# Optimization experiments

Measured on AMD Instinct MI355X. Metric: run time of the kernel, lower is better.

Reference implementation:

```python
import jax, jax.numpy as jnp
import numpy as np

B, S, V, H = 1, 2048, 1024, 16
D = V // H  # head_size = 64


def setup_inputs() -> dict:
    key = jax.random.key(0)
    ks = jax.random.split(key, 7)
    s = 1.0 / np.sqrt(V)  # keep logits in a sane range
    return {
        "x": jax.random.normal(ks[0], (B, S, V), jnp.float32),
        "W_qkv": (jax.random.normal(ks[1], (3 * V, V), jnp.float32) * s),
        "W_out": (jax.random.normal(ks[2], (V, V), jnp.float32) * s),
        "W_pos": (jax.random.normal(ks[3], (V, V), jnp.float32) * s),
        "u_vec": (jax.random.normal(ks[4], (1, H, 1, D), jnp.float32) * 0.02),
        "v_vec": (jax.random.normal(ks[5], (1, H, 1, D), jnp.float32) * 0.02),
        "rel_embed": jax.random.normal(ks[6], (S, V), jnp.float32),
    }


def reference(x, W_qkv, W_out, W_pos, u_vec, v_vec, rel_embed):
    b, s, _ = x.shape
    # qkv projection (nn.Linear, no bias): x @ W.T, then split into q,k,v
    qkv = x @ W_qkv.T
    q, k, v = jnp.split(qkv, 3, axis=-1)
    to_heads = lambda t: t.reshape(b, s, H, D).transpose(0, 2, 1, 3)  # [B,H,S,D]
    q, k, v = to_heads(q), to_heads(k), to_heads(v)

    # content term: (q + u) @ k^T  -> [B,H,S,S]
    attn_dots = jnp.einsum('bhid,bhjd->bhij', q + u_vec, k)

    # relative-position term: Linear(rel_embed).T viewed as [H, D, S]
    rel = (rel_embed @ W_pos.T).T.reshape(H, D, s)
    query_posn = jnp.einsum('bhid,hdj->bhij', q + v_vec, rel)  # [B,H,S,S]

    # Transformer-XL style shift-gather: out[i, j] = in[i, (j - i - 1) mod S]
    col_idx = ((-jnp.arange(s))[:, None] + jnp.arange(s)[None, :] - 1) % s
    shifted = jnp.take_along_axis(query_posn, col_idx[None, None, :, :], axis=-1)

    causal_mask = jnp.triu(jnp.ones((s, s), dtype=bool), k=1)  # True above diagonal
    dots = jnp.where(causal_mask, -jnp.inf, attn_dots + shifted) / np.sqrt(D)
    scores = jax.nn.softmax(dots, axis=-1)

    attn = jnp.einsum('bhij,bhjd->bhid', scores, v)
    out = attn.transpose(0, 2, 1, 3).reshape(b, s, V) @ W_out.T
    return out
```

## Files before the change

kernel.cpp:

```cpp
#include <hip/hip_runtime.h>
#include <math.h>

#define S 2048
#define H 16
#define D 64
#define V 1024

typedef float f32x4 __attribute__((ext_vector_type(4)));
typedef __bf16 bf16x8 __attribute__((ext_vector_type(8)));
typedef unsigned short u16;

#define GLOBAL_AS __attribute__((address_space(1)))
#define LDS_AS __attribute__((address_space(3)))

__device__ __forceinline__ u16 f2bf(float x) {
    unsigned u = __float_as_uint(x);
    u = u + 0x7FFFu + ((u >> 16) & 1u);
    return (u16)(u >> 16);
}
__device__ __forceinline__ float bf2f(u16 b) {
    return __uint_as_float(((unsigned)b) << 16);
}

#if __has_builtin(__builtin_amdgcn_global_load_lds)
#define HAS_ASYNC 1
#endif

__device__ __forceinline__ void async_ld16(const u16* g, u16* ldsu, int lane) {
#ifdef HAS_ASYNC
    auto gp = reinterpret_cast<GLOBAL_AS void*>(reinterpret_cast<uintptr_t>(g));
    auto lp = reinterpret_cast<LDS_AS void*>(reinterpret_cast<uintptr_t>(ldsu));
    __builtin_amdgcn_global_load_lds(gp, lp, 16, 0, 0);
#else
    *(uint4*)((char*)ldsu + lane * 16) = *(const uint4*)g;
#endif
}

__global__ __launch_bounds__(256) void prep5(
    const float* __restrict__ a0, u16* __restrict__ b0, int n0,
    const float* __restrict__ a1, u16* __restrict__ b1, int n1,
    const float* __restrict__ a2, u16* __restrict__ b2, int n2,
    const float* __restrict__ a3, u16* __restrict__ b3, int n3,
    const float* __restrict__ a4, u16* __restrict__ b4, int n4)
{
    const int tot = n0 + n1 + n2 + n3 + n4;
    for (int i = blockIdx.x * 256 + threadIdx.x; i < tot; i += gridDim.x * 256) {
        const float* s; u16* d; int j = i;
        if (j < n0) { s = a0; d = b0; }
        else if ((j -= n0) < n1) { s = a1; d = b1; }
        else if ((j -= n1) < n2) { s = a2; d = b2; }
        else if ((j -= n2) < n3) { s = a3; d = b3; }
        else { j -= n3; s = a4; d = b4; }
        float4 f = ((const float4*)s)[j];
        ((ushort4*)d)[j] = make_ushort4(f2bf(f.x), f2bf(f.y), f2bf(f.z), f2bf(f.w));
    }
}

__global__ __launch_bounds__(256) void gemm_proj(
    const u16* __restrict__ x_h, const u16* __restrict__ rel_h,
    const u16* __restrict__ Wq_h, const u16* __restrict__ Wpos_h,
    u16* __restrict__ qk_h, u16* __restrict__ Vt_g, u16* __restrict__ P_h)
{
    __shared__ u16 A_s[128 * 32];
    __shared__ u16 B_s[64 * 32];

    const int bid = blockIdx.x;
    const bool g1 = bid < 768;
    const int m0 = (g1 ? (bid / 48) : ((bid - 768) / 16)) * 128;
    const int n0 = (g1 ? (bid % 48) : ((bid - 768) % 16)) * 64;
    const u16* Ag = g1 ? x_h : rel_h;
    const u16* Bg = g1 ? Wq_h : Wpos_h;

    const int tid = threadIdx.x;
    const int lane = tid & 63;
    const int w = tid >> 6;
    const int wm = (w & 1) * 64, wn = (w >> 1) * 32;
    const int fr = lane & 15;
    const int fq = lane >> 4;
    const int lr = lane >> 2, lc = (lane & 3) * 8;

    f32x4 acc[4][2] = {};

    for (int k0 = 0; k0 < 1024; k0 += 32) {
        __syncthreads();
#pragma unroll
        for (int i = 0; i < 2; ++i) {
            const int r0 = w * 32 + i * 16;
            async_ld16(Ag + (size_t)(m0 + r0 + lr) * 1024 + k0 + lc, A_s + r0 * 32, lane);
        }
        async_ld16(Bg + (size_t)(n0 + w * 16 + lr) * 1024 + k0 + lc,
                   B_s + w * 16 * 32, lane);
        __syncthreads();

        bf16x8 a[4], b[2];
#pragma unroll
        for (int t = 0; t < 4; ++t)
            a[t] = *(const bf16x8*)&A_s[(wm + t * 16 + fr) * 32 + fq * 8];
#pragma unroll
        for (int t = 0; t < 2; ++t)
            b[t] = *(const bf16x8*)&B_s[(wn + t * 16 + fr) * 32 + fq * 8];
#pragma unroll
        for (int mi = 0; mi < 4; ++mi)
#pragma unroll
            for (int ni = 0; ni < 2; ++ni)
                acc[mi][ni] = __builtin_amdgcn_mfma_f32_16x16x32_bf16(
                    a[mi], b[ni], acc[mi][ni], 0, 0, 0);
    }

    const int er = fq * 4;
    if (g1 && n0 >= 2048) {
#pragma unroll
        for (int mi = 0; mi < 4; ++mi)
#pragma unroll
            for (int ni = 0; ni < 2; ++ni) {
                const int col = n0 - 2048 + wn + ni * 16 + fr;
                const int mrow = m0 + wm + mi * 16 + er;
                *(ushort4*)&Vt_g[(size_t)col * 2048 + mrow] = make_ushort4(
                    f2bf(acc[mi][ni][0]), f2bf(acc[mi][ni][1]),
                    f2bf(acc[mi][ni][2]), f2bf(acc[mi][ni][3]));
            }
    } else {
        u16* Cb = g1 ? qk_h : P_h;
        const int ldc = g1 ? 2048 : 1024;
#pragma unroll
        for (int mi = 0; mi < 4; ++mi)
#pragma unroll
            for (int ni = 0; ni < 2; ++ni)
#pragma unroll
                for (int g = 0; g < 4; ++g)
                    Cb[(size_t)(m0 + wm + mi * 16 + er + g) * ldc + n0 + wn + ni * 16 + fr] =
                        f2bf(acc[mi][ni][g]);
    }
}

__global__ __launch_bounds__(256, 3) void attn_mfma(
    const u16* __restrict__ qk_h, const u16* __restrict__ Vt_g,
    const u16* __restrict__ P_h,
    const float* __restrict__ u_vec, const float* __restrict__ v_vec,
    u16* __restrict__ O_h)
{
    const int h = blockIdx.y;
    const int tile = ((blockIdx.y >> 3) & 1) ? blockIdx.x : (gridDim.x - 1 - blockIdx.x);
    const int i0 = tile * 64;
    const int tid = threadIdx.x;
    const int lane = tid & 63;
    const int w = tid >> 6;
    const int fr = lane & 15;
    const int fq = lane >> 4;

    __shared__ u16 K_s[64 * 72];
    __shared__ u16 Vt_s[64 * 72];
    __shared__ u16 P_s[128 * 72];
    __shared__ u16 p_s[64 * 72];

    bf16x8 qu[2], qv[2];
    {
        const int row = i0 + w * 16 + fr;
        const int base = h * 64 + fq * 8;
#pragma unroll
        for (int c = 0; c < 2; ++c) {
            bf16x8 q8 = *(const bf16x8*)(qk_h + (size_t)row * 2048 + base + c * 32);
            float4 u0 = *(const float4*)(u_vec + base + c * 32);
            float4 u1 = *(const float4*)(u_vec + base + c * 32 + 4);
            float4 v0 = *(const float4*)(v_vec + base + c * 32);
            float4 v1 = *(const float4*)(v_vec + base + c * 32 + 4);
            const float uf[8] = {u0.x, u0.y, u0.z, u0.w, u1.x, u1.y, u1.z, u1.w};
            const float vf[8] = {v0.x, v0.y, v0.z, v0.w, v1.x, v1.y, v1.z, v1.w};
#pragma unroll
            for (int j = 0; j < 8; ++j) {
                const float qf = (float)q8[j];
                qu[c][j] = (__bf16)(qf + uf[j]);
                qv[c][j] = (__bf16)(qf + vf[j]);
            }
        }
    }

    const int rKV = tid >> 2;
    const int cKV = (tid & 3) * 16;
    const int rP = tid >> 1;
    const int cP = (tid & 1) * 32;

    uint4 pfK0, pfK1, pfV0, pfV1, pfP0, pfP1, pfP2, pfP3;
    auto load_pf = [&](int j0) {
        const u16* kg = qk_h + (size_t)(j0 + rKV) * 2048 + 1024 + h * 64 + cKV;
        pfK0 = *(const uint4*)kg;
        pfK1 = *(const uint4*)(kg + 8);
        const u16* vg = Vt_g + (size_t)(h * 64 + rKV) * 2048 + j0 + cKV;
        pfV0 = *(const uint4*)vg;
        pfV1 = *(const uint4*)(vg + 8);
        int prow = S + j0 - i0 - 64 + rP;
        if (prow > S - 1) prow = S - 1;
        const u16* pg = P_h + (size_t)prow * 1024 + h * 64 + cP;
        pfP0 = *(const uint4*)pg;
        pfP1 = *(const uint4*)(pg + 8);
        pfP2 = *(const uint4*)(pg + 16);
        pfP3 = *(const uint4*)(pg + 24);
    };

    f32x4 O[4] = {};
    float l[4] = {};

    const int tbase = 3 - w;
    const int bsh = 15 - fq * 4;

    load_pf(0);

    for (int j0 = 0; j0 <= i0; j0 += 64) {
        __syncthreads();
        *(uint4*)&K_s[rKV * 72 + cKV] = pfK0;
        *(uint4*)&K_s[rKV * 72 + cKV + 8] = pfK1;
        *(uint4*)&Vt_s[rKV * 72 + cKV] = pfV0;
        *(uint4*)&Vt_s[rKV * 72 + cKV + 8] = pfV1;
        *(uint4*)&P_s[rP * 72 + cP] = pfP0;
        *(uint4*)&P_s[rP * 72 + cP + 8] = pfP1;
        *(uint4*)&P_s[rP * 72 + cP + 16] = pfP2;
        *(uint4*)&P_s[rP * 72 + cP + 24] = pfP3;
        if (j0 + 64 <= i0) load_pf(j0 + 64);
        __syncthreads();

        f32x4 accQK[4] = {};
        f32x4 accQP[5] = {};
#pragma unroll
        for (int c = 0; c < 2; ++c) {
            const int kk = c * 32 + fq * 8;
#pragma unroll
            for (int nt = 0; nt < 4; ++nt) {
                bf16x8 b = *(const bf16x8*)&K_s[(nt * 16 + fr) * 72 + kk];
                accQK[nt] = __builtin_amdgcn_mfma_f32_16x16x32_bf16(qu[c], b, accQK[nt], 0, 0, 0);
            }
#pragma unroll
            for (int t = 0; t < 5; ++t) {
                bf16x8 b = *(const bf16x8*)&P_s[((tbase + t) * 16 + fr) * 72 + kk];
                accQP[t] = __builtin_amdgcn_mfma_f32_16x16x32_bf16(qv[c], b, accQP[t], 0, 0, 0);
            }
        }

        float p[4][4];
#pragma unroll
        for (int nt = 0; nt < 4; ++nt)
#pragma unroll
            for (int g = 0; g < 4; ++g) {
                const int b = bsh - g;
                const int srcfr = fr + b;
                const int srcLane = (fq << 4) | (srcfr & 15);
                const float lo = __shfl(accQP[nt][g], srcLane, 64);
                const float hi = __shfl(accQP[nt + 1][g], srcLane, 64);
                const float qp = (srcfr < 16) ? lo : hi;
                const int rr = w * 16 + fq * 4 + g;
                const int j = nt * 16 + fr;
                const float s = (accQK[nt][g] + qp) * 0.125f;
                const float e = ((j0 + j) <= (i0 + rr)) ? __expf(s) : 0.f;
                p[nt][g] = e;
                l[g] += e;
            }
#pragma unroll
        for (int nt = 0; nt < 4; ++nt)
#pragma unroll
            for (int g = 0; g < 4; ++g)
                p_s[(w * 16 + fq * 4 + g) * 72 + nt * 16 + fr] = f2bf(p[nt][g]);

#pragma unroll
        for (int c = 0; c < 2; ++c) {
            const int kk = c * 32 + fq * 8;
            bf16x8 a = *(const bf16x8*)&p_s[(w * 16 + fr) * 72 + kk];
#pragma unroll
            for (int nt = 0; nt < 4; ++nt) {
                bf16x8 b = *(const bf16x8*)&Vt_s[(nt * 16 + fr) * 72 + kk];
                O[nt] = __builtin_amdgcn_mfma_f32_16x16x32_bf16(a, b, O[nt], 0, 0, 0);
            }
        }
    }

#pragma unroll
    for (int g = 0; g < 4; ++g)
#pragma unroll
        for (int off = 1; off < 16; off <<= 1)
            l[g] += __shfl_xor(l[g], off, 64);

#pragma unroll
    for (int nt = 0; nt < 4; ++nt)
#pragma unroll
        for (int g = 0; g < 4; ++g) {
            const int rr = w * 16 + fq * 4 + g;
            O_h[(size_t)(i0 + rr) * 1024 + h * 64 + nt * 16 + fr] = f2bf(O[nt][g] / l[g]);
        }
}

__global__ __launch_bounds__(256) void gemm_out(
    const u16* __restrict__ O_g, const u16* __restrict__ Wout_h,
    float* __restrict__ C)
{
    __shared__ u16 A_s[64 * 32];
    __shared__ u16 B_s[64 * 32];

    const int tid = threadIdx.x;
    const int lane = tid & 63;
    const int w = tid >> 6;
    const int m0 = blockIdx.y * 64, n0 = blockIdx.x * 64;
    const int wm = (w & 1) * 32, wn = (w >> 1) * 32;
    const int fr = lane & 15;
    const int fq = lane >> 4;
    const int lr = lane >> 2, lc = (lane & 3) * 8;

    f32x4 acc[2][2] = {};

    for (int k0 = 0; k0 < 1024; k0 += 32) {
        __syncthreads();
        async_ld16(O_g + (size_t)(m0 + w * 16 + lr) * 1024 + k0 + lc,
                   A_s + w * 16 * 32, lane);
        async_ld16(Wout_h + (size_t)(n0 + w * 16 + lr) * 1024 + k0 + lc,
                   B_s + w * 16 * 32, lane);
        __syncthreads();

        bf16x8 a[2], b[2];
#pragma unroll
        for (int t = 0; t < 2; ++t) {
            a[t] = *(const bf16x8*)&A_s[(wm + t * 16 + fr) * 32 + fq * 8];
            b[t] = *(const bf16x8*)&B_s[(wn + t * 16 + fr) * 32 + fq * 8];
        }
#pragma unroll
        for (int mi = 0; mi < 2; ++mi)
#pragma unroll
            for (int ni = 0; ni < 2; ++ni)
                acc[mi][ni] = __builtin_amdgcn_mfma_f32_16x16x32_bf16(
                    a[mi], b[ni], acc[mi][ni], 0, 0, 0);
    }

    const int er = fq * 4;
#pragma unroll
    for (int mi = 0; mi < 2; ++mi)
#pragma unroll
        for (int ni = 0; ni < 2; ++ni)
#pragma unroll
            for (int g = 0; g < 4; ++g)
                C[(size_t)(m0 + wm + mi * 16 + er + g) * 1024 + n0 + wn + ni * 16 + fr] =
                    acc[mi][ni][g];
}

extern "C" void kernel_launch(void* const* d_in, const int* in_sizes, int n_in,
                              void* d_out, int out_size, void* d_ws, size_t ws_size,
                              hipStream_t stream) {
    const float* x     = (const float*)d_in[0];
    const float* W_qkv = (const float*)d_in[1];
    const float* W_out = (const float*)d_in[2];
    const float* W_pos = (const float*)d_in[3];
    const float* u_vec = (const float*)d_in[4];
    const float* v_vec = (const float*)d_in[5];
    const float* rel   = (const float*)d_in[6];
    float* out = (float*)d_out;

    char* ws = (char*)d_ws;
    u16* x_h    = (u16*)(ws);
    u16* rel_h  = (u16*)(ws + 4194304);
    u16* Wq_h   = (u16*)(ws + 8388608);
    u16* Wpos_h = (u16*)(ws + 14680064);
    u16* Wout_h = (u16*)(ws + 16777216);
    u16* qk_h   = (u16*)(ws + 18874368);
    u16* Vt_g   = (u16*)(ws + 27262976);
    u16* P_h    = (u16*)(ws + 31457280);
    u16* O_h    = (u16*)(ws + 35651584);

    prep5<<<dim3(2048), dim3(256), 0, stream>>>(
        x, x_h, 2048 * 1024 / 4,
        rel, rel_h, 2048 * 1024 / 4,
        W_qkv, Wq_h, 3072 * 1024 / 4,
        W_pos, Wpos_h, 1024 * 1024 / 4,
        W_out, Wout_h, 1024 * 1024 / 4);

    gemm_proj<<<dim3(1024), dim3(256), 0, stream>>>(
        x_h, rel_h, Wq_h, Wpos_h, qk_h, Vt_g, P_h);

    attn_mfma<<<dim3(32, 16), dim3(256), 0, stream>>>(
        qk_h, Vt_g, P_h, u_vec, v_vec, O_h);

    gemm_out<<<dim3(16, 32), dim3(256), 0, stream>>>(O_h, Wout_h, out);
}
```

Measured before the change: 195.1 us.

## Enlarge projection GEMM tiles with swizzled LDS and ring-buffer P rows in attention

```diff
diff --git a/kernel.cpp b/kernel.cpp
--- a/kernel.cpp
+++ b/kernel.cpp
@@ -61,50 +61,53 @@
     const u16* __restrict__ Wq_h, const u16* __restrict__ Wpos_h,
     u16* __restrict__ qk_h, u16* __restrict__ Vt_g, u16* __restrict__ P_h)
 {
-    __shared__ u16 A_s[128 * 32];
-    __shared__ u16 B_s[64 * 32];
+    __shared__ u16 A_s[128 * 64];
+    __shared__ u16 B_s[128 * 64];
 
     const int bid = blockIdx.x;
-    const bool g1 = bid < 768;
-    const int m0 = (g1 ? (bid / 48) : ((bid - 768) / 16)) * 128;
-    const int n0 = (g1 ? (bid % 48) : ((bid - 768) % 16)) * 64;
+    const bool g1 = bid < 384;
+    const int m0 = (g1 ? (bid / 24) : ((bid - 384) / 8)) * 128;
+    const int n0 = (g1 ? (bid % 24) : ((bid - 384) % 8)) * 128;
     const u16* Ag = g1 ? x_h : rel_h;
     const u16* Bg = g1 ? Wq_h : Wpos_h;
 
     const int tid = threadIdx.x;
     const int lane = tid & 63;
     const int w = tid >> 6;
-    const int wm = (w & 1) * 64, wn = (w >> 1) * 32;
+    const int wm = (w & 1) * 64, wn = (w >> 1) * 64;
     const int fr = lane & 15;
     const int fq = lane >> 4;
-    const int lr = lane >> 2, lc = (lane & 3) * 8;
-
-    f32x4 acc[4][2] = {};
-
-    for (int k0 = 0; k0 < 1024; k0 += 32) {
-        __syncthreads();
-#pragma unroll
-        for (int i = 0; i < 2; ++i) {
-            const int r0 = w * 32 + i * 16;
-            async_ld16(Ag + (size_t)(m0 + r0 + lr) * 1024 + k0 + lc, A_s + r0 * 32, lane);
-        }
-        async_ld16(Bg + (size_t)(n0 + w * 16 + lr) * 1024 + k0 + lc,
-                   B_s + w * 16 * 32, lane);
-        __syncthreads();
-
-        bf16x8 a[4], b[2];
-#pragma unroll
-        for (int t = 0; t < 4; ++t)
-            a[t] = *(const bf16x8*)&A_s[(wm + t * 16 + fr) * 32 + fq * 8];
-#pragma unroll
-        for (int t = 0; t < 2; ++t)
-            b[t] = *(const bf16x8*)&B_s[(wn + t * 16 + fr) * 32 + fq * 8];
-#pragma unroll
-        for (int mi = 0; mi < 4; ++mi)
-#pragma unroll
-            for (int ni = 0; ni < 2; ++ni)
-                acc[mi][ni] = __builtin_amdgcn_mfma_f32_16x16x32_bf16(
-                    a[mi], b[ni], acc[mi][ni], 0, 0, 0);
+    const int sr = lane >> 3;
+    const int scl = ((lane & 7) ^ sr) * 8;
+
+    f32x4 acc[4][4] = {};
+
+    for (int k0 = 0; k0 < 1024; k0 += 64) {
+        __syncthreads();
+#pragma unroll
+        for (int i = 0; i < 4; ++i) {
+            const int r0 = w * 32 + i * 8;
+            async_ld16(Ag + (size_t)(m0 + r0 + sr) * 1024 + k0 + scl, A_s + r0 * 64, lane);
+            async_ld16(Bg + (size_t)(n0 + r0 + sr) * 1024 + k0 + scl, B_s + r0 * 64, lane);
+        }
+        __syncthreads();
+
+#pragma unroll
+        for (int c = 0; c < 2; ++c) {
+            const int ps = ((c * 4 + fq) ^ (fr & 7)) * 8;
+            bf16x8 a[4], b[4];
+#pragma unroll
+            for (int t = 0; t < 4; ++t) {
+                a[t] = *(const bf16x8*)&A_s[(wm + t * 16 + fr) * 64 + ps];
+                b[t] = *(const bf16x8*)&B_s[(wn + t * 16 + fr) * 64 + ps];
+            }
+#pragma unroll
+            for (int mi = 0; mi < 4; ++mi)
+#pragma unroll
+                for (int ni = 0; ni < 4; ++ni)
+                    acc[mi][ni] = __builtin_amdgcn_mfma_f32_16x16x32_bf16(
+                        a[mi], b[ni], acc[mi][ni], 0, 0, 0);
+        }
     }
 
     const int er = fq * 4;
@@ -112,7 +115,7 @@
 #pragma unroll
         for (int mi = 0; mi < 4; ++mi)
 #pragma unroll
-            for (int ni = 0; ni < 2; ++ni) {
+            for (int ni = 0; ni < 4; ++ni) {
                 const int col = n0 - 2048 + wn + ni * 16 + fr;
                 const int mrow = m0 + wm + mi * 16 + er;
                 *(ushort4*)&Vt_g[(size_t)col * 2048 + mrow] = make_ushort4(
@@ -125,7 +128,7 @@
 #pragma unroll
         for (int mi = 0; mi < 4; ++mi)
 #pragma unroll
-            for (int ni = 0; ni < 2; ++ni)
+            for (int ni = 0; ni < 4; ++ni)
 #pragma unroll
                 for (int g = 0; g < 4; ++g)
                     Cb[(size_t)(m0 + wm + mi * 16 + er + g) * ldc + n0 + wn + ni * 16 + fr] =
@@ -177,10 +180,10 @@
 
     const int rKV = tid >> 2;
     const int cKV = (tid & 3) * 16;
-    const int rP = tid >> 1;
-    const int cP = (tid & 1) * 32;
-
-    uint4 pfK0, pfK1, pfV0, pfV1, pfP0, pfP1, pfP2, pfP3;
+    const int rP = tid >> 2;
+    const int cP = (tid & 3) * 16;
+
+    uint4 pfK0, pfK1, pfV0, pfV1, pfP0, pfP1;
     auto load_pf = [&](int j0) {
         const u16* kg = qk_h + (size_t)(j0 + rKV) * 2048 + 1024 + h * 64 + cKV;
         pfK0 = *(const uint4*)kg;
@@ -188,14 +191,20 @@
         const u16* vg = Vt_g + (size_t)(h * 64 + rKV) * 2048 + j0 + cKV;
         pfV0 = *(const uint4*)vg;
         pfV1 = *(const uint4*)(vg + 8);
-        int prow = S + j0 - i0 - 64 + rP;
+        int prow = S + j0 - i0 + rP;
         if (prow > S - 1) prow = S - 1;
         const u16* pg = P_h + (size_t)prow * 1024 + h * 64 + cP;
         pfP0 = *(const uint4*)pg;
         pfP1 = *(const uint4*)(pg + 8);
-        pfP2 = *(const uint4*)(pg + 16);
-        pfP3 = *(const uint4*)(pg + 24);
     };
+
+    {
+        const int prow = S - i0 - 64 + rP;
+        const u16* pg = P_h + (size_t)prow * 1024 + h * 64 + cP;
+        u16* dst = &P_s[(prow & 127) * 72 + cP];
+        *(uint4*)dst = *(const uint4*)pg;
+        *(uint4*)(dst + 8) = *(const uint4*)(pg + 8);
+    }
 
     f32x4 O[4] = {};
     float l[4] = {};
@@ -211,13 +220,15 @@
         *(uint4*)&K_s[rKV * 72 + cKV + 8] = pfK1;
         *(uint4*)&Vt_s[rKV * 72 + cKV] = pfV0;
         *(uint4*)&Vt_s[rKV * 72 + cKV + 8] = pfV1;
-        *(uint4*)&P_s[rP * 72 + cP] = pfP0;
-        *(uint4*)&P_s[rP * 72 + cP + 8] = pfP1;
-        *(uint4*)&P_s[rP * 72 + cP + 16] = pfP2;
-        *(uint4*)&P_s[rP * 72 + cP + 24] = pfP3;
+        {
+            const int prp = (S + j0 - i0 + rP) & 127;
+            *(uint4*)&P_s[prp * 72 + cP] = pfP0;
+            *(uint4*)&P_s[prp * 72 + cP + 8] = pfP1;
+        }
         if (j0 + 64 <= i0) load_pf(j0 + 64);
         __syncthreads();
 
+        const int wb = S + j0 - i0 - 64;
         f32x4 accQK[4] = {};
         f32x4 accQP[5] = {};
 #pragma unroll
@@ -230,7 +241,8 @@
             }
 #pragma unroll
             for (int t = 0; t < 5; ++t) {
-                bf16x8 b = *(const bf16x8*)&P_s[((tbase + t) * 16 + fr) * 72 + kk];
+                const int phys = (wb + (tbase + t) * 16 + fr) & 127;
+                bf16x8 b = *(const bf16x8*)&P_s[phys * 72 + kk];
                 accQP[t] = __builtin_amdgcn_mfma_f32_16x16x32_bf16(qv[c], b, accQP[t], 0, 0, 0);
             }
         }
@@ -241,11 +253,9 @@
 #pragma unroll
             for (int g = 0; g < 4; ++g) {
                 const int b = bsh - g;
-                const int srcfr = fr + b;
-                const int srcLane = (fq << 4) | (srcfr & 15);
-                const float lo = __shfl(accQP[nt][g], srcLane, 64);
-                const float hi = __shfl(accQP[nt + 1][g], srcLane, 64);
-                const float qp = (srcfr < 16) ? lo : hi;
+                const int srcLane = (fq << 4) | ((fr + b) & 15);
+                const float sv = (fr >= b) ? accQP[nt][g] : accQP[nt + 1][g];
+                const float qp = __shfl(sv, srcLane, 64);
                 const int rr = w * 16 + fq * 4 + g;
                 const int j = nt * 16 + fr;
                 const float s = (accQK[nt][g] + qp) * 0.125f;
@@ -367,7 +377,7 @@
         W_pos, Wpos_h, 1024 * 1024 / 4,
         W_out, Wout_h, 1024 * 1024 / 4);
 
-    gemm_proj<<<dim3(1024), dim3(256), 0, stream>>>(
+    gemm_proj<<<dim3(512), dim3(256), 0, stream>>>(
         x_h, rel_h, Wq_h, Wpos_h, qk_h, Vt_g, P_h);
 
     attn_mfma<<<dim3(32, 16), dim3(256), 0, stream>>>(
```

After: 196.7 us. No clear change (+0.8%).
